# Kernel tuning notes

Measured on AMD Instinct MI355X. Metric: run time of the kernel, lower is better.

The kernel has to match this reference:

```python
import jax, jax.numpy as jnp
import numpy as np

B, L, K, D = 1, 4096, 24, 512


def setup_inputs() -> dict:
    key = jax.random.key(0)
    k1, k2, k3, k4 = jax.random.split(key, 4)
    u = jax.random.normal(k1, (B, L, D), dtype=jnp.float32)
    # spectral filter bank (learned parameter initialized from Hankel eigenvectors in the
    # original; random init is equivalent for a correctness baseline), scaled ~O(1/sqrt(L))
    filters = jax.random.normal(k2, (L, K), dtype=jnp.float32) * (1.0 / np.sqrt(L))
    M_phi_plus = jax.random.normal(k3, (K, D, D), dtype=jnp.float32) * (1.0 / np.sqrt(K * D))
    M_phi_minus = jax.random.normal(k4, (K, D, D), dtype=jnp.float32) * (1.0 / np.sqrt(K * D))
    return {"u": u, "filters": filters, "M_phi_plus": M_phi_plus, "M_phi_minus": M_phi_minus}


def _causal_conv(u, phi):
    # Causal linear convolution of every input channel with every spectral filter via FFT.
    # u: [B, L, D], phi: [L, K] -> [B, L, K, D]
    L_ = u.shape[1]
    n = 2 * L_  # zero-pad so circular FFT conv == linear causal conv
    Uf = jnp.fft.rfft(u, n=n, axis=1)                    # [B, F, D]
    Pf = jnp.fft.rfft(phi, n=n, axis=0)                  # [F, K]
    prod = Uf[:, :, None, :] * Pf[None, :, :, None]      # [B, F, K, D]
    return jnp.fft.irfft(prod, n=n, axis=1)[:, :L_]      # [B, L, K, D]


def reference(u, filters, M_phi_plus, M_phi_minus):
    L_ = u.shape[1]
    # sgn[t] = (-1)^t ; U_minus[b,l,k,d] = sum_s u[b,s,d] * phi[l-s,k] * (-1)^(l-s),
    # which equals convolving with the alternating-sign filter phi[t]*(-1)^t
    # (the original implements this as sgn-pre/post-multiplication around FlashFFTConv).
    sgn = jnp.where(jnp.arange(L_) % 2 == 0, 1.0, -1.0).astype(u.dtype)
    U_plus = _causal_conv(u, filters)                      # [B, L, K, D]
    U_minus = _causal_conv(u, filters * sgn[:, None])      # [B, L, K, D]
    y = (jnp.einsum('blkd,kdo->blo', U_plus, M_phi_plus)
         + jnp.einsum('blkd,kdo->blo', U_minus, M_phi_minus))
    return y
```

## Files before the change

kernel.cpp:

```cpp
#include <hip/hip_runtime.h>
#include <hip/hip_bf16.h>
#include <cstdint>
#include <cstddef>

using bf16 = __hip_bfloat16;

typedef __attribute__((ext_vector_type(4))) float f32x4;
typedef __attribute__((ext_vector_type(8))) short s16x8;

#define LSEQ 4096
#define DDIM 512
#define KFLT 24
#define NFFT 8192
#define MR 8192

__device__ __forceinline__ void gld16(const bf16* g, bf16* l) {
  __builtin_amdgcn_global_load_lds((const __attribute__((address_space(1))) void*)g,
                                   (__attribute__((address_space(3))) void*)l, 16, 0, 0);
}

#define MEMFENCE asm volatile("" ::: "memory")
#define BAR() do { MEMFENCE; __builtin_amdgcn_s_barrier(); MEMFENCE; } while (0)

__device__ __forceinline__ float fsin_rev(float rev) {
  float s; asm("v_sin_f32 %0, %1" : "=v"(s) : "v"(rev)); return s;
}
__device__ __forceinline__ float fcos_rev(float rev) {
  float c; asm("v_cos_f32 %0, %1" : "=v"(c) : "v"(rev)); return c;
}

__device__ __forceinline__ void stage16(const bf16* g, int ldk, bf16* ldsbase,
                                        int wave, int lane) {
  const int r8 = lane >> 3;
  const int sc = ((lane & 7) ^ r8) * 8;
  gld16(g + (size_t)(wave * 8 + r8) * ldk + sc, ldsbase + wave * 512);
}

__device__ __forceinline__ s16x8 ldfrag(const bf16* buf, int row, int kk, int l4) {
  return *(const s16x8*)(buf + row * 64 + (((kk * 4 + l4) ^ (row & 7)) * 8));
}

__global__ __launch_bounds__(256) void transpose_cast(
    const float* __restrict__ in, bf16* __restrict__ out, int R, int C) {
  __shared__ float tile[32][33];
  const size_t bo = (size_t)blockIdx.z * R * C;
  const float* inb = in + bo;
  bf16* outb = out + bo;
  int c0 = blockIdx.x * 32, r0 = blockIdx.y * 32;
  int tx = threadIdx.x & 31, ty = threadIdx.x >> 5;
  #pragma unroll
  for (int i = 0; i < 32; i += 8)
    tile[ty + i][tx] = inb[(size_t)(r0 + ty + i) * C + (c0 + tx)];
  __syncthreads();
  #pragma unroll
  for (int i = 0; i < 32; i += 8)
    outb[(size_t)(c0 + ty + i) * R + (r0 + tx)] = __float2bfloat16(tile[tx][ty + i]);
}

__global__ __launch_bounds__(256) void add2_cast(
    const bf16* __restrict__ P, bf16* __restrict__ out) {
  size_t i = ((size_t)blockIdx.x * 256 + threadIdx.x) * 8;
  const size_t MN = (size_t)MR * DDIM;
  s16x8 a = *(const s16x8*)(P + i);
  s16x8 b = *(const s16x8*)(P + i + MN);
  bf16 o[8];
  #pragma unroll
  for (int e = 0; e < 8; ++e) {
    float fa = __uint_as_float((unsigned)(unsigned short)a[e] << 16);
    float fb = __uint_as_float((unsigned)(unsigned short)b[e] << 16);
    o[e] = __float2bfloat16(fa + fb);
  }
  *(s16x8*)(out + i) = *(const s16x8*)o;
}

__global__ __launch_bounds__(256) void tr_reduce4(
    const float* __restrict__ S, bf16* __restrict__ out) {
  __shared__ float tile[32][33];
  int c0 = blockIdx.x * 32, r0 = blockIdx.y * 32;
  int tx = threadIdx.x & 31, ty = threadIdx.x >> 5;
  const int nt = c0 >> 8;
  const int scl = (c0 & 255) + tx;
  const size_t SB = (size_t)MR * 256;
  #pragma unroll
  for (int i = 0; i < 32; i += 8) {
    size_t ro = (size_t)(r0 + ty + i) * 256 + scl;
    tile[ty + i][tx] = S[(0 * 2 + nt) * SB + ro] + S[(1 * 2 + nt) * SB + ro] +
                       S[(2 * 2 + nt) * SB + ro] + S[(3 * 2 + nt) * SB + ro];
  }
  __syncthreads();
  #pragma unroll
  for (int i = 0; i < 32; i += 8)
    out[(size_t)(c0 + ty + i) * MR + (r0 + tx)] = __float2bfloat16(tile[tx][ty + i]);
}

__global__ __launch_bounds__(256) void reduce4y(
    const float* __restrict__ P, const float* __restrict__ vnyq,
    float* __restrict__ y) {
  size_t i = ((size_t)blockIdx.x * 256 + threadIdx.x) * 4;
  const size_t MN = (size_t)LSEQ * DDIM;
  int l = (int)(i >> 9), o = (int)(i & 511);
  f32x4 a = *(const f32x4*)(P + i);
  f32x4 b = *(const f32x4*)(P + i + MN);
  f32x4 c = *(const f32x4*)(P + i + 2 * MN);
  f32x4 d = *(const f32x4*)(P + i + 3 * MN);
  f32x4 v = *(const f32x4*)(vnyq + o);
  float sg = (l & 1) ? -(1.f / NFFT) : (1.f / NFFT);
  f32x4 r = a + b + c + d;
  r[0] += sg * v[0]; r[1] += sg * v[1]; r[2] += sg * v[2]; r[3] += sg * v[3];
  *(f32x4*)(y + i) = r;
}

__global__ __launch_bounds__(256) void compute_pf(
    const float* __restrict__ phi, float* __restrict__ Pf) {
  int f0 = blockIdx.x * 2;
  int tid = threadIdx.x;
  int lane = tid & 63, wave = tid >> 6;
  float pre[2][KFLT], pim[2][KFLT];
  #pragma unroll
  for (int ff = 0; ff < 2; ++ff)
    #pragma unroll
    for (int k = 0; k < KFLT; ++k) { pre[ff][k] = 0.f; pim[ff][k] = 0.f; }
  for (int cch = 0; cch < LSEQ / 256; ++cch) {
    int t = cch * 256 + tid;
    const float4* pv = (const float4*)(phi + (size_t)t * KFLT);
    float4 v0 = pv[0], v1 = pv[1], v2 = pv[2], v3 = pv[3], v4 = pv[4], v5 = pv[5];
    float pr[KFLT] = {v0.x, v0.y, v0.z, v0.w, v1.x, v1.y, v1.z, v1.w,
                      v2.x, v2.y, v2.z, v2.w, v3.x, v3.y, v3.z, v3.w,
                      v4.x, v4.y, v4.z, v4.w, v5.x, v5.y, v5.z, v5.w};
    #pragma unroll
    for (int ff = 0; ff < 2; ++ff) {
      int m = ((f0 + ff) * t) & (NFFT - 1);
      float rev = (float)m * (1.f / NFFT);
      float s = fsin_rev(rev), c = fcos_rev(rev);
      #pragma unroll
      for (int k = 0; k < KFLT; ++k) {
        pre[ff][k] += pr[k] * c;
        pim[ff][k] -= pr[k] * s;
      }
    }
  }
  __shared__ float red[4][2][2 * KFLT];
  #pragma unroll
  for (int ff = 0; ff < 2; ++ff)
    #pragma unroll
    for (int k = 0; k < KFLT; ++k) {
      float r = pre[ff][k], i2 = pim[ff][k];
      #pragma unroll
      for (int off = 32; off > 0; off >>= 1) {
        r += __shfl_down(r, off, 64);
        i2 += __shfl_down(i2, off, 64);
      }
      if (lane == 0) { red[wave][ff][2 * k] = r; red[wave][ff][2 * k + 1] = i2; }
    }
  __syncthreads();
  if (tid < 96) {
    int ff = tid / 48, q = tid % 48;
    int f = f0 + ff;
    if (f <= NFFT / 2)
      Pf[(size_t)f * 48 + q] =
          red[0][ff][q] + red[1][ff][q] + red[2][ff][q] + red[3][ff][q];
  }
}

__global__ __launch_bounds__(256) void build_pw(
    const float* __restrict__ Pf, float* __restrict__ Pw, float* __restrict__ wnyq) {
  int idx = blockIdx.x * 256 + threadIdx.x;
  int j = idx >> 12, f = idx & 4095;
  float re, im;
  if (j < KFLT) {
    re = Pf[(size_t)f * 48 + j * 2];
    im = Pf[(size_t)f * 48 + j * 2 + 1];
  } else {
    int k = j - KFLT, g = NFFT / 2 - f;
    re = Pf[(size_t)g * 48 + k * 2];
    im = -Pf[(size_t)g * 48 + k * 2 + 1];
  }
  Pw[(size_t)idx * 2] = re;
  Pw[(size_t)idx * 2 + 1] = im;
  if (idx < 48)
    wnyq[idx] = (idx < KFLT) ? Pf[(size_t)(NFFT / 2) * 48 + idx * 2]
                             : Pf[(idx - KFLT) * 2];
}

__global__ __launch_bounds__(256) void nyq_u(
    const float* __restrict__ u, float* __restrict__ Unyq) {
  int d = blockIdx.x * 256 + threadIdx.x;
  int t0 = blockIdx.y * 64;
  float acc = 0.f;
  for (int t = t0; t < t0 + 64; t += 2)
    acc += u[(size_t)t * DDIM + d] - u[(size_t)(t + 1) * DDIM + d];
  atomicAdd(&Unyq[d], acc);
}

__global__ __launch_bounds__(256) void vnyq_k(
    const bf16* __restrict__ Mt, const float* __restrict__ Unyq,
    const float* __restrict__ wnyq, float* __restrict__ vnyq) {
  __shared__ float us[DDIM];
  int j = blockIdx.x, tid = threadIdx.x;
  us[tid] = Unyq[tid];
  us[tid + 256] = Unyq[tid + 256];
  __syncthreads();
  float w = wnyq[j];
  int o = blockIdx.y * 128 + (tid >> 1);
  int dh = (tid & 1) * 256;
  const bf16* row = Mt + ((size_t)j * DDIM + o) * DDIM + dh;
  float acc = 0.f;
  for (int d0 = 0; d0 < 256; d0 += 8) {
    s16x8 v = *(const s16x8*)(row + d0);
    #pragma unroll
    for (int e = 0; e < 8; ++e)
      acc += us[dh + d0 + e] * __uint_as_float((unsigned)(unsigned short)v[e] << 16);
  }
  acc += __shfl_xor(acc, 1, 64);
  if ((tid & 1) == 0) atomicAdd(&vnyq[o], w * acc);
}

template <int STORE>
__global__ __launch_bounds__(1024, 4) void gemmG(
    const bf16* __restrict__ Bt, int ldk,
    bf16* __restrict__ Obf, float* __restrict__ Of) {
  __shared__ bf16 sA[3 * 128 * 64];
  __shared__ bf16 sB[3 * 256 * 64];

  const int lin = blockIdx.x;
  const int wid = (lin & 7) * 32 + (lin >> 3);

  int mt, nt, kt0, nkt, ks;
  if constexpr (STORE == 0) {
    ks = wid >> 7; int rem = wid & 127; mt = rem >> 1; nt = rem & 1;
    kt0 = ks * 32; nkt = 32;
  } else {
    ks = wid >> 6; int rem = wid & 63; mt = rem >> 1; nt = rem & 1;
    kt0 = ks * 32; nkt = 32;
  }

  const int tid = threadIdx.x, lane = tid & 63, wave = tid >> 6;
  const int l15 = lane & 15, l4 = lane >> 4;
  const int wr = wave >> 2, wc = wave & 3;
  const int r8 = lane >> 3, c8 = lane & 7;
  const int mtile = mt * 128, ntile = nt * 256;
  const bf16* Bb = Bt + (size_t)ntile * ldk;

  f32x4 acc[2][4];
  #pragma unroll
  for (int m = 0; m < 2; ++m)
    #pragma unroll
    for (int n = 0; n < 4; ++n) acc[m][n] = f32x4{0.f, 0.f, 0.f, 0.f};

  auto genA = [&](int t, int buf) {
    const int kbase = (kt0 + t) * 64 + ((c8 ^ r8) * 8);
    const int row = mtile + wave * 8 + r8;
    bf16 o[8];
    if constexpr (STORE == 0) {
      const int f = row >> 1;
      const bool odd = row & 1;
      #pragma unroll
      for (int e = 0; e < 8; ++e) {
        int m = (f * (kbase + e)) & (NFFT - 1);
        float rev = (float)m * (1.f / NFFT);
        o[e] = __float2bfloat16(odd ? -fsin_rev(rev) : fcos_rev(rev));
      }
    } else {
      #pragma unroll
      for (int e = 0; e < 8; ++e) {
        int r = kbase + e;
        int f = r >> 1;
        int m = (f * row) & (NFFT - 1);
        float rev = (float)m * (1.f / NFFT);
        float sc2 = ((f == 0) ? 1.f : 2.f) * (1.f / NFFT);
        o[e] = __float2bfloat16((r & 1) ? -sc2 * fsin_rev(rev)
                                        : sc2 * fcos_rev(rev));
      }
    }
    *(s16x8*)(sA + buf * (128 * 64) + (wave * 8 + r8) * 64 + c8 * 8) =
        *(const s16x8*)o;
  };
  auto stageB = [&](int t, int buf) {
    const size_t ko = (size_t)(kt0 + t) * 64;
    stage16(Bb + ko, ldk, sB + buf * (256 * 64), wave, lane);
    stage16(Bb + (size_t)128 * ldk + ko, ldk, sB + buf * (256 * 64) + 128 * 64,
            wave, lane);
  };

  genA(0, 0);
  genA(1, 1);
  stageB(0, 0);
  stageB(1, 1);
  asm volatile("s_waitcnt vmcnt(2)" ::: "memory");
  asm volatile("s_waitcnt lgkmcnt(0)" ::: "memory");
  BAR();

  for (int t = 0; t < nkt; ++t) {
    const int buf = t % 3;
    const bf16* bA = sA + buf * (128 * 64);
    const bf16* bB = sB + buf * (256 * 64);
    const bool i2 = (t + 2 < nkt);

    s16x8 afr[2][2], bfr[4][2];
    #pragma unroll
    for (int n = 0; n < 4; ++n)
      #pragma unroll
      for (int kk = 0; kk < 2; ++kk)
        bfr[n][kk] = ldfrag(bB, wc * 64 + n * 16 + l15, kk, l4);
    #pragma unroll
    for (int m = 0; m < 2; ++m)
      #pragma unroll
      for (int kk = 0; kk < 2; ++kk)
        afr[m][kk] = ldfrag(bA, wr * 32 + m * 16 + l15, kk, l4);

    if (i2) {
      genA(t + 2, (t + 2) % 3);
      stageB(t + 2, (t + 2) % 3);
    }

    __builtin_amdgcn_s_setprio(1);
    #pragma unroll
    for (int m = 0; m < 2; ++m)
      #pragma unroll
      for (int n = 0; n < 4; ++n)
        #pragma unroll
        for (int kk = 0; kk < 2; ++kk)
          acc[m][n] = __builtin_amdgcn_mfma_f32_16x16x32_bf16(
              afr[m][kk], bfr[n][kk], acc[m][n], 0, 0, 0);
    __builtin_amdgcn_s_setprio(0);

    if (i2) { asm volatile("s_waitcnt vmcnt(2)" ::: "memory"); }
    else    { asm volatile("s_waitcnt vmcnt(0)" ::: "memory"); }
    asm volatile("s_waitcnt lgkmcnt(0)" ::: "memory");
    BAR();
  }

  #pragma unroll
  for (int m = 0; m < 2; ++m)
    #pragma unroll
    for (int n = 0; n < 4; ++n)
      #pragma unroll
      for (int e = 0; e < 4; ++e) {
        int row = mtile + wr * 32 + m * 16 + l4 * 4 + e;
        int col = ntile + wc * 64 + n * 16 + l15;
        if constexpr (STORE == 0)
          Obf[(size_t)ks * MR * DDIM + (size_t)row * DDIM + col] =
              __float2bfloat16(acc[m][n][e]);
        else
          Of[(size_t)ks * LSEQ * DDIM + (size_t)row * DDIM + col] = acc[m][n][e];
      }
}

__global__ __launch_bounds__(1024, 4) void gemmW(
    const bf16* __restrict__ Auf, const bf16* __restrict__ Mt,
    const float* __restrict__ Pw, float* __restrict__ Slots) {
  __shared__ bf16 sB[3 * 256 * 64];
  __shared__ bf16 sA[256 * 64];
  __shared__ float2 sW[12 * 128];

  const int lin = blockIdx.x;
  const int q = lin & 7;
  const int pos = lin >> 3;
  const int jg = q >> 1, mhalf = q & 1;
  const int nt = pos >> 4;
  const int mt = mhalf * 16 + (pos & 15);

  const int tid = threadIdx.x, lane = tid & 63, wave = tid >> 6;
  const int l15 = lane & 15, l4 = lane >> 4;
  const int wr = wave >> 1, wc = wave & 1;

  float* dst = Slots + (size_t)(jg * 2 + nt) * ((size_t)MR * 256);

  f32x4 acc[2][8];
  #pragma unroll
  for (int m = 0; m < 2; ++m)
    #pragma unroll
    for (int n = 0; n < 8; ++n) acc[m][n] = f32x4{0.f, 0.f, 0.f, 0.f};

  auto stageB_ = [&](int s) {
    const int j = jg * 12 + (s % 12), kt = s / 12;
    const bf16* bb = Mt + (size_t)j * (DDIM * DDIM) + (size_t)(nt * 256) * DDIM + kt * 64;
    bf16* db = sB + (s % 3) * (256 * 64);
    stage16(bb, DDIM, db, wave, lane);
    stage16(bb + (size_t)128 * DDIM, DDIM, db + 128 * 64, wave, lane);
  };
  auto stageA_ = [&](int kt) {
    const bf16* ab = Auf + (size_t)(mt * 256) * DDIM + kt * 64;
    stage16(ab, DDIM, sA, wave, lane);
    stage16(ab + (size_t)128 * DDIM, DDIM, sA + 128 * 64, wave, lane);
  };

  for (int idx = tid; idx < 1536; idx += 1024) {
    int jj2 = idx >> 7, fo = idx & 127;
    sW[idx] = *(const float2*)(Pw +
        (((size_t)(jg * 12 + jj2)) * 4096 + (size_t)mt * 128 + fo) * 2);
  }
  stageB_(0);
  stageB_(1);
  stageA_(0);
  asm volatile("s_waitcnt vmcnt(0) lgkmcnt(0)" ::: "memory");
  BAR();

  int4 selfA[2][2];

  for (int s = 0; s < 96; ++s) {
    const int jj = s % 12, kt = s / 12;
    const bf16* bB = sB + (s % 3) * (256 * 64);

    if (s) {
      if (s == 95) { asm volatile("s_waitcnt vmcnt(0)" ::: "memory"); }
      else         { asm volatile("s_waitcnt vmcnt(2)" ::: "memory"); }
      BAR();
    }
    if (s + 2 < 96) stageB_(s + 2);
    if (jj == 6 && kt < 7) stageA_(kt + 1);

    if (jj == 0) {
      #pragma unroll
      for (int m = 0; m < 2; ++m)
        #pragma unroll
        for (int kk = 0; kk < 2; ++kk) {
          s16x8 v = ldfrag(sA, wr * 32 + m * 16 + l15, kk, l4);
          selfA[m][kk] = *(const int4*)&v;
        }
    }

    float wx[2], swy[2];
    #pragma unroll
    for (int m = 0; m < 2; ++m) {
      int fr = (wr * 32 + m * 16 + l15) >> 1;
      float2 w = sW[jj * 128 + fr];
      wx[m] = w.x;
      swy[m] = (l15 & 1) ? w.y : -w.y;
    }

    #pragma unroll
    for (int kk = 0; kk < 2; ++kk) {
      s16x8 afr[2];
      #pragma unroll
      for (int m = 0; m < 2; ++m) {
        const int4 sv = selfA[m][kk];
        int4 pv;
        pv.x = __builtin_amdgcn_mov_dpp(sv.x, 0xB1, 0xF, 0xF, true);
        pv.y = __builtin_amdgcn_mov_dpp(sv.y, 0xB1, 0xF, 0xF, true);
        pv.z = __builtin_amdgcn_mov_dpp(sv.z, 0xB1, 0xF, 0xF, true);
        pv.w = __builtin_amdgcn_mov_dpp(sv.w, 0xB1, 0xF, 0xF, true);
        const int sp[4] = {sv.x, sv.y, sv.z, sv.w};
        const int pp[4] = {pv.x, pv.y, pv.z, pv.w};
        bf16 ob[8];
        #pragma unroll
        for (int t2 = 0; t2 < 4; ++t2) {
          float fsl = __uint_as_float((unsigned)sp[t2] << 16);
          float fsh = __uint_as_float((unsigned)sp[t2] & 0xffff0000u);
          float fpl = __uint_as_float((unsigned)pp[t2] << 16);
          float fph = __uint_as_float((unsigned)pp[t2] & 0xffff0000u);
          ob[2 * t2]     = __float2bfloat16(wx[m] * fsl + swy[m] * fpl);
          ob[2 * t2 + 1] = __float2bfloat16(wx[m] * fsh + swy[m] * fph);
        }
        afr[m] = *(const s16x8*)ob;
      }
      #pragma unroll
      for (int nh = 0; nh < 2; ++nh) {
        s16x8 bfr[4];
        #pragma unroll
        for (int n = 0; n < 4; ++n)
          bfr[n] = ldfrag(bB, wc * 128 + (nh * 4 + n) * 16 + l15, kk, l4);
        __builtin_amdgcn_s_setprio(1);
        #pragma unroll
        for (int m = 0; m < 2; ++m)
          #pragma unroll
          for (int n = 0; n < 4; ++n)
            acc[m][nh * 4 + n] = __builtin_amdgcn_mfma_f32_16x16x32_bf16(
                afr[m], bfr[n], acc[m][nh * 4 + n], 0, 0, 0);
        __builtin_amdgcn_s_setprio(0);
      }
    }
  }

  #pragma unroll
  for (int m = 0; m < 2; ++m)
    #pragma unroll
    for (int n = 0; n < 8; ++n)
      #pragma unroll
      for (int e = 0; e < 4; ++e) {
        int row = mt * 256 + wr * 32 + m * 16 + l4 * 4 + e;
        int col = wc * 128 + n * 16 + l15;
        dst[(size_t)row * 256 + col] = acc[m][n][e];
      }
}

#define WS_W     0ULL
#define WS_AUF   67108864ULL
#define WS_UT    75497472ULL
#define WS_MT    79691776ULL
#define WS_PF    104857600ULL
#define WS_PW    105644288ULL
#define WS_WNYQ  107217152ULL
#define WS_UNYQ  107217408ULL
#define WS_VNYQ  107219456ULL
#define WS_YBT   107221504ULL
#define WS_G1P   115610112ULL
#define WS_TOTAL 132387328ULL

extern "C" void kernel_launch(void* const* d_in, const int* in_sizes, int n_in,
                              void* d_out, int out_size, void* d_ws, size_t ws_size,
                              hipStream_t stream) {
  const float* u   = (const float*)d_in[0];
  const float* phi = (const float*)d_in[1];
  const float* Mp  = (const float*)d_in[2];
  const float* Mm  = (const float*)d_in[3];
  float* y = (float*)d_out;

  if (ws_size < WS_TOTAL) return;

  char* ws = (char*)d_ws;
  float* Slots= (float*)(ws + WS_W);
  bf16*  Auf  = (bf16*)(ws + WS_AUF);
  bf16*  uT   = (bf16*)(ws + WS_UT);
  bf16*  Mt   = (bf16*)(ws + WS_MT);
  float* Pf   = (float*)(ws + WS_PF);
  float* Pw   = (float*)(ws + WS_PW);
  float* wny  = (float*)(ws + WS_WNYQ);
  float* Uny  = (float*)(ws + WS_UNYQ);
  float* vny  = (float*)(ws + WS_VNYQ);
  bf16*  Ybt  = (bf16*)(ws + WS_YBT);
  bf16*  G1P  = (bf16*)(ws + WS_G1P);
  float* G3P  = (float*)(ws + WS_AUF);

  transpose_cast<<<dim3(16, 128, 1), 256, 0, stream>>>(u, uT, LSEQ, DDIM);
  transpose_cast<<<dim3(16, 16, 24), 256, 0, stream>>>(Mp, Mt, DDIM, DDIM);
  transpose_cast<<<dim3(16, 16, 24), 256, 0, stream>>>(Mm, Mt + (size_t)24 * DDIM * DDIM,
                                                       DDIM, DDIM);
  compute_pf<<<dim3(2049), 256, 0, stream>>>(phi, Pf);
  build_pw<<<dim3(48 * 4096 / 256), 256, 0, stream>>>(Pf, Pw, wny);
  hipMemsetAsync(Uny, 0, DDIM * sizeof(float), stream);
  nyq_u<<<dim3(2, 64), 256, 0, stream>>>(u, Uny);

  gemmG<0><<<256, 1024, 0, stream>>>(uT, LSEQ, G1P, nullptr);
  add2_cast<<<dim3(MR * DDIM / 2048), 256, 0, stream>>>(G1P, Auf);

  gemmW<<<256, 1024, 0, stream>>>(Auf, Mt, Pw, Slots);

  tr_reduce4<<<dim3(16, 256), 256, 0, stream>>>(Slots, Ybt);
  hipMemsetAsync(vny, 0, DDIM * sizeof(float), stream);
  vnyq_k<<<dim3(48, 4), 256, 0, stream>>>(Mt, Uny, wny, vny);

  gemmG<1><<<256, 1024, 0, stream>>>(Ybt, MR, nullptr, G3P);
  reduce4y<<<dim3(LSEQ * DDIM / 1024), 256, 0, stream>>>(G3P, vny, y);
}
```

Measured before the change: 477.4 us.

## Halve gemmW N-tile to 128, use 512-thread blocks, load A fragments directly

```diff
diff --git a/kernel.cpp b/kernel.cpp
--- a/kernel.cpp
+++ b/kernel.cpp
@@ -27,6 +27,17 @@
 }
 __device__ __forceinline__ float fcos_rev(float rev) {
   float c; asm("v_cos_f32 %0, %1" : "=v"(c) : "v"(rev)); return c;
+}
+
+__device__ __forceinline__ void stage_half(const bf16* g, int ldk, bf16* ldsbase,
+                                           int wave, int lane) {
+  const int r8 = lane >> 3;
+  const int sc = ((lane & 7) ^ r8) * 8;
+  #pragma unroll
+  for (int q = 0; q < 2; ++q) {
+    const int c = wave * 2 + q;
+    gld16(g + (size_t)(c * 8 + r8) * ldk + sc, ldsbase + c * 512);
+  }
 }
 
 __device__ __forceinline__ void stage16(const bf16* g, int ldk, bf16* ldsbase,
@@ -78,14 +89,14 @@
   __shared__ float tile[32][33];
   int c0 = blockIdx.x * 32, r0 = blockIdx.y * 32;
   int tx = threadIdx.x & 31, ty = threadIdx.x >> 5;
-  const int nt = c0 >> 8;
-  const int scl = (c0 & 255) + tx;
-  const size_t SB = (size_t)MR * 256;
+  const int nt = c0 >> 7;
+  const int scl = (c0 & 127) + tx;
+  const size_t SB = (size_t)MR * 128;
   #pragma unroll
   for (int i = 0; i < 32; i += 8) {
-    size_t ro = (size_t)(r0 + ty + i) * 256 + scl;
-    tile[ty + i][tx] = S[(0 * 2 + nt) * SB + ro] + S[(1 * 2 + nt) * SB + ro] +
-                       S[(2 * 2 + nt) * SB + ro] + S[(3 * 2 + nt) * SB + ro];
+    size_t ro = (size_t)(r0 + ty + i) * 128 + scl;
+    tile[ty + i][tx] = S[(0 * 4 + nt) * SB + ro] + S[(1 * 4 + nt) * SB + ro] +
+                       S[(2 * 4 + nt) * SB + ro] + S[(3 * 4 + nt) * SB + ro];
   }
   __syncthreads();
   #pragma unroll
@@ -346,11 +357,10 @@
       }
 }
 
-__global__ __launch_bounds__(1024, 4) void gemmW(
+__global__ __launch_bounds__(512, 4) void gemmW(
     const bf16* __restrict__ Auf, const bf16* __restrict__ Mt,
     const float* __restrict__ Pw, float* __restrict__ Slots) {
-  __shared__ bf16 sB[3 * 256 * 64];
-  __shared__ bf16 sA[256 * 64];
+  __shared__ bf16 sB[3 * 128 * 64];
   __shared__ float2 sW[12 * 128];
 
   const int lin = blockIdx.x;
@@ -362,68 +372,65 @@
 
   const int tid = threadIdx.x, lane = tid & 63, wave = tid >> 6;
   const int l15 = lane & 15, l4 = lane >> 4;
-  const int wr = wave >> 1, wc = wave & 1;
-
-  float* dst = Slots + (size_t)(jg * 2 + nt) * ((size_t)MR * 256);
+
+  float* dst = Slots + (size_t)(jg * 4 + nt) * ((size_t)MR * 128);
 
   f32x4 acc[2][8];
   #pragma unroll
   for (int m = 0; m < 2; ++m)
     #pragma unroll
     for (int n = 0; n < 8; ++n) acc[m][n] = f32x4{0.f, 0.f, 0.f, 0.f};
+
+  int4 selfA[2][2];
 
   auto stageB_ = [&](int s) {
     const int j = jg * 12 + (s % 12), kt = s / 12;
-    const bf16* bb = Mt + (size_t)j * (DDIM * DDIM) + (size_t)(nt * 256) * DDIM + kt * 64;
-    bf16* db = sB + (s % 3) * (256 * 64);
-    stage16(bb, DDIM, db, wave, lane);
-    stage16(bb + (size_t)128 * DDIM, DDIM, db + 128 * 64, wave, lane);
+    const bf16* bb = Mt + (size_t)j * (DDIM * DDIM) + (size_t)(nt * 128) * DDIM + kt * 64;
+    stage_half(bb, DDIM, sB + (s % 3) * (128 * 64), wave, lane);
   };
-  auto stageA_ = [&](int kt) {
-    const bf16* ab = Auf + (size_t)(mt * 256) * DDIM + kt * 64;
-    stage16(ab, DDIM, sA, wave, lane);
-    stage16(ab + (size_t)128 * DDIM, DDIM, sA + 128 * 64, wave, lane);
+  auto loadA = [&](int kt) {
+    #pragma unroll
+    for (int m = 0; m < 2; ++m)
+      #pragma unroll
+      for (int kk = 0; kk < 2; ++kk) {
+        const int row = mt * 256 + wave * 32 + m * 16 + l15;
+        selfA[m][kk] = *(const int4*)(Auf + (size_t)row * DDIM + kt * 64 +
+                                      (kk * 4 + l4) * 8);
+      }
   };
 
-  for (int idx = tid; idx < 1536; idx += 1024) {
+  #pragma unroll
+  for (int t = 0; t < 3; ++t) {
+    int idx = tid * 3 + t;
     int jj2 = idx >> 7, fo = idx & 127;
     sW[idx] = *(const float2*)(Pw +
         (((size_t)(jg * 12 + jj2)) * 4096 + (size_t)mt * 128 + fo) * 2);
   }
+  loadA(0);
   stageB_(0);
   stageB_(1);
-  stageA_(0);
   asm volatile("s_waitcnt vmcnt(0) lgkmcnt(0)" ::: "memory");
   BAR();
 
-  int4 selfA[2][2];
-
   for (int s = 0; s < 96; ++s) {
     const int jj = s % 12, kt = s / 12;
-    const bf16* bB = sB + (s % 3) * (256 * 64);
+    const bf16* bB = sB + (s % 3) * (128 * 64);
 
     if (s) {
       if (s == 95) { asm volatile("s_waitcnt vmcnt(0)" ::: "memory"); }
       else         { asm volatile("s_waitcnt vmcnt(2)" ::: "memory"); }
       BAR();
     }
+    if (jj == 0 && s) loadA(kt);
     if (s + 2 < 96) stageB_(s + 2);
-    if (jj == 6 && kt < 7) stageA_(kt + 1);
-
-    if (jj == 0) {
-      #pragma unroll
-      for (int m = 0; m < 2; ++m)
-        #pragma unroll
-        for (int kk = 0; kk < 2; ++kk) {
-          s16x8 v = ldfrag(sA, wr * 32 + m * 16 + l15, kk, l4);
-          selfA[m][kk] = *(const int4*)&v;
-        }
+    if (jj == 0 && s) {
+      asm volatile("s_waitcnt vmcnt(2)" ::: "memory");
     }
 
     float wx[2], swy[2];
     #pragma unroll
     for (int m = 0; m < 2; ++m) {
-      int fr = (wr * 32 + m * 16 + l15) >> 1;
+      int fr = (wave * 32 + m * 16 + l15) >> 1;
       float2 w = sW[jj * 128 + fr];
       wx[m] = w.x;
       swy[m] = (l15 & 1) ? w.y : -w.y;
@@ -459,7 +466,7 @@
         s16x8 bfr[4];
         #pragma unroll
         for (int n = 0; n < 4; ++n)
-          bfr[n] = ldfrag(bB, wc * 128 + (nh * 4 + n) * 16 + l15, kk, l4);
+          bfr[n] = ldfrag(bB, (nh * 4 + n) * 16 + l15, kk, l4);
         __builtin_amdgcn_s_setprio(1);
         #pragma unroll
         for (int m = 0; m < 2; ++m)
@@ -478,9 +485,9 @@
     for (int n = 0; n < 8; ++n)
       #pragma unroll
       for (int e = 0; e < 4; ++e) {
-        int row = mt * 256 + wr * 32 + m * 16 + l4 * 4 + e;
-        int col = wc * 128 + n * 16 + l15;
-        dst[(size_t)row * 256 + col] = acc[m][n][e];
+        int row = mt * 256 + wave * 32 + m * 16 + l4 * 4 + e;
+        int col = n * 16 + l15;
+        dst[(size_t)row * 128 + col] = acc[m][n][e];
       }
 }
 
@@ -534,7 +541,7 @@
   gemmG<0><<<256, 1024, 0, stream>>>(uT, LSEQ, G1P, nullptr);
   add2_cast<<<dim3(MR * DDIM / 2048), 256, 0, stream>>>(G1P, Auf);
 
-  gemmW<<<256, 1024, 0, stream>>>(Auf, Mt, Pw, Slots);
+  gemmW<<<512, 512, 0, stream>>>(Auf, Mt, Pw, Slots);
 
   tr_reduce4<<<dim3(16, 256), 256, 0, stream>>>(Slots, Ybt);
   hipMemsetAsync(vny, 0, DDIM * sizeof(float), stream);
```

Result: slower. 813.6 us (+70.4%).
